# Performance work log

Measured on AMD Instinct MI355X. Metric: run time of the kernel, lower is better.

## Reference

```python
import jax, jax.numpy as jnp
import numpy as np

B, S, P, D = 32, 128, 64, 256   # batch, seq_len, pad_size, input_size
H, NF = 128, 3                   # hidden_size, n_filters
BI = 2                           # bidirectional -> b=2
OUT = 2                          # output_size
INITRANGE = 0.05


def setup_inputs() -> dict:
    key = jax.random.key(0)
    ks = jax.random.split(key, 17)
    u = lambda k, shape: jax.random.uniform(k, shape, jnp.float32, -INITRANGE, INITRANGE)
    return {
        "inputs": jax.random.normal(ks[0], (B, S, P, D), jnp.float32),
        "inputs_demoip": jax.random.normal(ks[1], (B, 3), jnp.float32),
        # Conv1d(1,1,kernel=D) collapses to a single dot product + scalar bias
        "conv_w": u(ks[2], (D,)),
        "conv_b": u(ks[3], ()),
        # Conv1d(1,NF,kernel=H*BI) collapses to NF dot products + bias
        "conv2_w": u(ks[4], (NF, H * BI)),
        "conv2_b": u(ks[5], (NF,)),
        # GRU params, forward and backward directions (PyTorch gate order r,z,n)
        "W_ih_f": u(ks[6], (3 * H, D)),
        "W_hh_f": u(ks[7], (3 * H, H)),
        "b_ih_f": u(ks[8], (3 * H,)),
        "b_hh_f": u(ks[9], (3 * H,)),
        "W_ih_b": u(ks[10], (3 * H, D)),
        "W_hh_b": u(ks[11], (3 * H, H)),
        "b_ih_b": u(ks[12], (3 * H,)),
        "b_hh_b": u(ks[13], (3 * H,)),
        "lin_w": u(ks[14], (OUT, H * BI * NF + 3)),
        "lin_b": u(ks[15], (OUT,)),
        "batch_size": B,
    }


def _gru_dir(x_seq, W_ih, W_hh, b_ih, b_hh, reverse):
    """Single-direction GRU, PyTorch semantics. x_seq: [B,S,D] -> [B,S,H]."""
    xg = jnp.einsum('bsd,gd->bsg', x_seq, W_ih) + b_ih  # [B,S,3H] precomputed input gates

    def step(h, xg_t):
        hg = h @ W_hh.T + b_hh
        xr, xz, xn = jnp.split(xg_t, 3, axis=-1)
        hr, hz, hn = jnp.split(hg, 3, axis=-1)
        r = jax.nn.sigmoid(xr + hr)
        z = jax.nn.sigmoid(xz + hz)
        n = jnp.tanh(xn + r * hn)
        h_new = (1.0 - z) * n + z * h
        return h_new, h_new

    h0 = jnp.zeros((x_seq.shape[0], W_hh.shape[1]), x_seq.dtype)
    _, hs = jax.lax.scan(step, h0, jnp.swapaxes(xg, 0, 1), reverse=reverse)
    return jnp.swapaxes(hs, 0, 1)


def reference(inputs, inputs_demoip, conv_w, conv_b, conv2_w, conv2_b,
              W_ih_f, W_hh_f, b_ih_f, b_hh_f,
              W_ih_b, W_hh_b, b_ih_b, b_hh_b,
              lin_w, lin_b, batch_size):
    # --- convolutional attention pooling over pad dim (fused, no per-step loop) ---
    scores = jnp.einsum('bspd,d->bsp', inputs, conv_w) + conv_b      # [B,S,P]
    conv_wts = jax.nn.softmax(scores, axis=-1)                        # [B,S,P]
    convolutions = jnp.einsum('bsp,bspd->bsd', conv_wts, inputs)      # [B,S,D]
    # --- bidirectional GRU (eval mode: dropout is identity) ---
    hf = _gru_dir(convolutions, W_ih_f, W_hh_f, b_ih_f, b_hh_f, False)
    hb = _gru_dir(convolutions, W_ih_b, W_hh_b, b_ih_b, b_hh_b, True)
    states_rnn = jnp.concatenate([hf, hb], axis=-1)                   # [B,S,2H]
    # --- second attention (conv2 over states, softmax over time per filter) ---
    alpha_scores = jnp.einsum('bsh,fh->bfs', states_rnn, conv2_w) + conv2_b[None, :, None]
    alpha = jax.nn.softmax(alpha_scores, axis=-1)                     # [B,NF,S]
    context = jnp.einsum('bfs,bsh->bfh', alpha, states_rnn).reshape(states_rnn.shape[0], -1)
    context_v2 = jnp.concatenate([context, inputs_demoip], axis=1)    # [B, 2H*NF+3]
    out = jax.nn.softmax(context_v2 @ lin_w.T + lin_b, axis=-1)       # [B,OUT]
    return out, alpha, states_rnn, context, conv_wts
```

## Files before the change

kernel.cpp:

```cpp
#include <hip/hip_runtime.h>
#include <hip/hip_bf16.h>

#define BB 32
#define SS 128
#define PP 64
#define DD 256
#define HH 128
#define NF 3


__global__ __launch_bounds__(256) void k_pool(
    const float* __restrict__ inp,
    const float* __restrict__ conv_w,
    const float* __restrict__ conv_bp,
    float* __restrict__ conv_out,
    float* __restrict__ conv_wts_out)
{
    __shared__ float scores[PP];
    __shared__ float wts[PP];
    __shared__ float4 part4[256];

    const int bs   = blockIdx.x;
    const int t    = threadIdx.x;
    const int lane = t & 63;
    const int wv   = t >> 6;

    const float4* src = reinterpret_cast<const float4*>(inp + (size_t)bs * (PP * DD));
    const float4  cw  = reinterpret_cast<const float4*>(conv_w)[lane];
    const float   cb  = conv_bp[0];

    float4 v[16];
#pragma unroll
    for (int i = 0; i < 16; ++i) v[i] = src[i * 256 + t];

    float part[16];
#pragma unroll
    for (int i = 0; i < 16; ++i)
        part[i] = v[i].x * cw.x + v[i].y * cw.y + v[i].z * cw.z + v[i].w * cw.w;

#pragma unroll
    for (int i = 0; i < 16; ++i) {
#pragma unroll
        for (int m = 32; m >= 1; m >>= 1) part[i] += __shfl_xor(part[i], m);
        if (lane == i) scores[i * 4 + wv] = part[i] + cb;
    }
    __syncthreads();

    if (wv == 0) {
        float s = scores[lane];
        float mx = s;
#pragma unroll
        for (int m = 32; m >= 1; m >>= 1) mx = fmaxf(mx, __shfl_xor(mx, m));
        float e = __expf(s - mx);
        float sm = e;
#pragma unroll
        for (int m = 32; m >= 1; m >>= 1) sm += __shfl_xor(sm, m);
        float w = e / sm;
        wts[lane] = w;
        conv_wts_out[(size_t)bs * PP + lane] = w;
    }
    __syncthreads();

    float4 acc = {0.f, 0.f, 0.f, 0.f};
#pragma unroll
    for (int i = 0; i < 16; ++i) {
        const float w = wts[4 * i + wv];
        acc.x = fmaf(w, v[i].x, acc.x);
        acc.y = fmaf(w, v[i].y, acc.y);
        acc.z = fmaf(w, v[i].z, acc.z);
        acc.w = fmaf(w, v[i].w, acc.w);
    }
    part4[t] = acc;
    __syncthreads();

    if (wv == 0) {
        float4 a = part4[lane];
        const float4 b1 = part4[64 + lane];
        const float4 b2 = part4[128 + lane];
        const float4 b3 = part4[192 + lane];
        a.x += b1.x + b2.x + b3.x;
        a.y += b1.y + b2.y + b3.y;
        a.z += b1.z + b2.z + b3.z;
        a.w += b1.w + b2.w + b3.w;
        reinterpret_cast<float4*>(conv_out + (size_t)bs * DD)[lane] = a;
    }
}

#define GBM 128
#define GBN 128
#define GBK 32
#define GAS 132

__global__ __launch_bounds__(256) void k_xg(
    const float* __restrict__ A,
    const float* __restrict__ Wf,
    const float* __restrict__ Wb,
    const float* __restrict__ bf,
    const float* __restrict__ bb,
    float* __restrict__ xg)
{
    __shared__ float as_[GBK * GAS];
    __shared__ float bs_[GBK * GAS];

    const int t  = threadIdx.x;
    const int i0 = blockIdx.x * GBM;
    const int j0 = blockIdx.y * GBN;
    const int tx = t & 15, ty = t >> 4;

    const float* Wsrc = (j0 < 384) ? (Wf + (size_t)j0 * DD) : (Wb + (size_t)(j0 - 384) * DD);
    const float* bsrc = (j0 < 384) ? (bf + j0) : (bb + (j0 - 384));

    float acc[8][8];
#pragma unroll
    for (int ii = 0; ii < 8; ++ii)
#pragma unroll
        for (int jj = 0; jj < 8; ++jj) acc[ii][jj] = 0.f;

    float4 pa[4], pb[4];
#pragma unroll
    for (int p = 0; p < 4; ++p) {
        const int idx = p * 256 + t, r = idx >> 3, k4 = idx & 7;
        pa[p] = *reinterpret_cast<const float4*>(&A[(size_t)(i0 + r) * DD + k4 * 4]);
        pb[p] = *reinterpret_cast<const float4*>(&Wsrc[(size_t)r * DD + k4 * 4]);
    }

    for (int kt = 0; kt < DD; kt += GBK) {
#pragma unroll
        for (int p = 0; p < 4; ++p) {
            const int idx = p * 256 + t, r = idx >> 3, k4 = idx & 7;
            as_[(k4 * 4 + 0) * GAS + r] = pa[p].x;
            as_[(k4 * 4 + 1) * GAS + r] = pa[p].y;
            as_[(k4 * 4 + 2) * GAS + r] = pa[p].z;
            as_[(k4 * 4 + 3) * GAS + r] = pa[p].w;
            bs_[(k4 * 4 + 0) * GAS + r] = pb[p].x;
            bs_[(k4 * 4 + 1) * GAS + r] = pb[p].y;
            bs_[(k4 * 4 + 2) * GAS + r] = pb[p].z;
            bs_[(k4 * 4 + 3) * GAS + r] = pb[p].w;
        }
        __syncthreads();
        if (kt + GBK < DD) {
#pragma unroll
            for (int p = 0; p < 4; ++p) {
                const int idx = p * 256 + t, r = idx >> 3, k4 = idx & 7;
                pa[p] = *reinterpret_cast<const float4*>(&A[(size_t)(i0 + r) * DD + kt + GBK + k4 * 4]);
                pb[p] = *reinterpret_cast<const float4*>(&Wsrc[(size_t)r * DD + kt + GBK + k4 * 4]);
            }
        }
#pragma unroll 8
        for (int k = 0; k < GBK; ++k) {
            float a[8], bq[8];
            *reinterpret_cast<float4*>(&a[0])  = *reinterpret_cast<const float4*>(&as_[k * GAS + ty * 8]);
            *reinterpret_cast<float4*>(&a[4])  = *reinterpret_cast<const float4*>(&as_[k * GAS + ty * 8 + 4]);
            *reinterpret_cast<float4*>(&bq[0]) = *reinterpret_cast<const float4*>(&bs_[k * GAS + tx * 4]);
            *reinterpret_cast<float4*>(&bq[4]) = *reinterpret_cast<const float4*>(&bs_[k * GAS + 64 + tx * 4]);
#pragma unroll
            for (int ii = 0; ii < 8; ++ii)
#pragma unroll
                for (int jj = 0; jj < 8; ++jj) acc[ii][jj] += a[ii] * bq[jj];
        }
        __syncthreads();
    }

    float bias[8];
#pragma unroll
    for (int jj = 0; jj < 4; ++jj) {
        bias[jj]     = bsrc[tx * 4 + jj];
        bias[4 + jj] = bsrc[64 + tx * 4 + jj];
    }
#pragma unroll
    for (int ii = 0; ii < 8; ++ii) {
        float* dst = &xg[(size_t)(i0 + ty * 8 + ii) * 768 + j0];
        float4 o0, o1;
        o0.x = acc[ii][0] + bias[0]; o0.y = acc[ii][1] + bias[1];
        o0.z = acc[ii][2] + bias[2]; o0.w = acc[ii][3] + bias[3];
        o1.x = acc[ii][4] + bias[4]; o1.y = acc[ii][5] + bias[5];
        o1.z = acc[ii][6] + bias[6]; o1.w = acc[ii][7] + bias[7];
        reinterpret_cast<float4*>(dst + tx * 4)[0]      = o0;
        reinterpret_cast<float4*>(dst + 64 + tx * 4)[0] = o1;
    }
}

__device__ __forceinline__ float sigm(float x) { return 1.f / (1.f + __expf(-x)); }
__device__ __forceinline__ float tanh_f(float x) { return 2.f / (1.f + __expf(-2.f * x)) - 1.f; }

template<int CTRL>
__device__ __forceinline__ float dpp_mov(float x) {
    return __int_as_float(__builtin_amdgcn_update_dpp(
        0, __float_as_int(x), CTRL, 0xF, 0xF, true));
}
#define DPP_XOR1 0xB1
#define DPP_XOR2 0x4E
#define DPP_HMIR 0x141

#define HSEG16 20
#define CH 16
#define XROW 384

__global__ __launch_bounds__(512) void k_gru(
    const float* __restrict__ xg,
    const float* __restrict__ Whf,
    const float* __restrict__ Whb,
    const float* __restrict__ bhf,
    const float* __restrict__ bhb,
    const float* __restrict__ c2w,
    float* __restrict__ states,
    float* __restrict__ sc_part)
{
    const int blk = blockIdx.x;
    const int b   = blk >> 1;
    const int dir = blk & 1;
    const int tid = threadIdx.x;
    const int g   = tid >> 3;
    const int p   = tid & 7;

    __shared__ float hb[2][8 * HSEG16];
    __shared__ float xs[2][CH * XROW];
    __shared__ float sring[2][CH][HH];

    const float* Wh = dir ? Whb : Whf;
    const float* bh = dir ? bhb : bhf;

    const int j = g + 64 * ((p >> 2) & 1);
    const bool gate = (p & 3) == 0;
    float bhr = 0.f, bhz = 0.f, bhn = 0.f;
    if (gate) { bhr = bh[j]; bhz = bh[HH + j]; bhn = bh[2 * HH + j]; }

    float4 wra[4], wrb[4], wza[4], wzb[4], wna[4], wnb[4];
    {
        const float4* p_ra = reinterpret_cast<const float4*>(Wh + (size_t)g * HH + p * 16);
        const float4* p_rb = reinterpret_cast<const float4*>(Wh + (size_t)(g + 64) * HH + p * 16);
        const float4* p_za = reinterpret_cast<const float4*>(Wh + (size_t)(HH + g) * HH + p * 16);
        const float4* p_zb = reinterpret_cast<const float4*>(Wh + (size_t)(HH + g + 64) * HH + p * 16);
        const float4* p_na = reinterpret_cast<const float4*>(Wh + (size_t)(2 * HH + g) * HH + p * 16);
        const float4* p_nb = reinterpret_cast<const float4*>(Wh + (size_t)(2 * HH + g + 64) * HH + p * 16);
#pragma unroll
        for (int k = 0; k < 4; ++k) {
            wra[k] = p_ra[k]; wrb[k] = p_rb[k];
            wza[k] = p_za[k]; wzb[k] = p_zb[k];
            wna[k] = p_na[k]; wnb[k] = p_nb[k];
        }
    }

    const float* xg_bd = xg + (size_t)b * SS * 768 + dir * 384;
    const int hidx = (j >> 4) * HSEG16 + (j & 15);

    float4 pf[3];
#pragma unroll
    for (int j3 = 0; j3 < 3; ++j3) {
        const int flat4 = j3 * 512 + tid;
        const int sic = flat4 / 96, w4 = flat4 % 96;
        const int s = dir ? (SS - 1 - sic) : sic;
        pf[j3] = *reinterpret_cast<const float4*>(xg_bd + (size_t)s * 768 + w4 * 4);
    }
#pragma unroll
    for (int j3 = 0; j3 < 3; ++j3) {
        const int flat4 = j3 * 512 + tid;
        const int sic = flat4 / 96, w4 = flat4 % 96;
        *reinterpret_cast<float4*>(&xs[0][sic * XROW + w4 * 4]) = pf[j3];
    }
    if (tid < 8 * HSEG16) hb[0][tid] = 0.f;
    __syncthreads();
#pragma unroll
    for (int j3 = 0; j3 < 3; ++j3) {
        const int flat4 = j3 * 512 + tid;
        const int sic = flat4 / 96, w4 = flat4 % 96;
        const int stp = CH + sic;
        const int s = dir ? (SS - 1 - stp) : stp;
        pf[j3] = *reinterpret_cast<const float4*>(xg_bd + (size_t)s * 768 + w4 * 4);
    }

    for (int step = 0; step < SS; ++step) {
        const int cur = step & 1;
        const int sic = step & (CH - 1);
        const int buf = (step >> 4) & 1;

        const float* hrow = hb[cur];
        float4 hq[4];
#pragma unroll
        for (int k = 0; k < 4; ++k)
            hq[k] = *reinterpret_cast<const float4*>(&hrow[p * HSEG16 + k * 4]);

        float hp = 0.f, xrv = 0.f, xzv = 0.f, xnv = 0.f;
        if (gate) {
            hp  = hrow[hidx];
            xrv = xs[buf][sic * XROW + j];
            xzv = xs[buf][sic * XROW + HH + j];
            xnv = xs[buf][sic * XROW + 2 * HH + j];
        }

        float a_ra = 0.f, a_rb = 0.f, a_za = 0.f, a_zb = 0.f, a_na = 0.f, a_nb = 0.f;
#pragma unroll
        for (int k = 0; k < 4; ++k) {
            const float4 h4 = hq[k];
            a_ra = fmaf(wra[k].x, h4.x, a_ra); a_ra = fmaf(wra[k].y, h4.y, a_ra);
            a_ra = fmaf(wra[k].z, h4.z, a_ra); a_ra = fmaf(wra[k].w, h4.w, a_ra);
            a_rb = fmaf(wrb[k].x, h4.x, a_rb); a_rb = fmaf(wrb[k].y, h4.y, a_rb);
            a_rb = fmaf(wrb[k].z, h4.z, a_rb); a_rb = fmaf(wrb[k].w, h4.w, a_rb);
            a_za = fmaf(wza[k].x, h4.x, a_za); a_za = fmaf(wza[k].y, h4.y, a_za);
            a_za = fmaf(wza[k].z, h4.z, a_za); a_za = fmaf(wza[k].w, h4.w, a_za);
            a_zb = fmaf(wzb[k].x, h4.x, a_zb); a_zb = fmaf(wzb[k].y, h4.y, a_zb);
            a_zb = fmaf(wzb[k].z, h4.z, a_zb); a_zb = fmaf(wzb[k].w, h4.w, a_zb);
            a_na = fmaf(wna[k].x, h4.x, a_na); a_na = fmaf(wna[k].y, h4.y, a_na);
            a_na = fmaf(wna[k].z, h4.z, a_na); a_na = fmaf(wna[k].w, h4.w, a_na);
            a_nb = fmaf(wnb[k].x, h4.x, a_nb); a_nb = fmaf(wnb[k].y, h4.y, a_nb);
            a_nb = fmaf(wnb[k].z, h4.z, a_nb); a_nb = fmaf(wnb[k].w, h4.w, a_nb);
        }

        const bool own_b = (tid & 4) != 0;
        const float s_r = own_b ? a_ra : a_rb;
        const float s_z = own_b ? a_za : a_zb;
        const float s_n = own_b ? a_na : a_nb;
        float f_r = (own_b ? a_rb : a_ra) + dpp_mov<DPP_HMIR>(s_r);
        float f_z = (own_b ? a_zb : a_za) + dpp_mov<DPP_HMIR>(s_z);
        float f_n = (own_b ? a_nb : a_na) + dpp_mov<DPP_HMIR>(s_n);
        f_r += dpp_mov<DPP_XOR1>(f_r);
        f_z += dpp_mov<DPP_XOR1>(f_z);
        f_n += dpp_mov<DPP_XOR1>(f_n);
        f_r += dpp_mov<DPP_XOR2>(f_r);
        f_z += dpp_mov<DPP_XOR2>(f_z);
        f_n += dpp_mov<DPP_XOR2>(f_n);

        if (gate) {
            const float r = sigm(xrv + f_r + bhr);
            const float z = sigm(xzv + f_z + bhz);
            const float n = tanh_f(xnv + r * (f_n + bhn));
            const float hnew = (1.f - z) * n + z * hp;
            hb[cur ^ 1][hidx] = hnew;
            sring[buf][sic][j] = hnew;
        }

        if (sic == CH - 1 && step != SS - 1) {
#pragma unroll
            for (int j3 = 0; j3 < 3; ++j3) {
                const int flat4 = j3 * 512 + tid;
                const int sc = flat4 / 96, w4 = flat4 % 96;
                *reinterpret_cast<float4*>(&xs[buf ^ 1][sc * XROW + w4 * 4]) = pf[j3];
            }
        }
        __syncthreads();

        if (sic == CH - 1) {
            const int cb = (step >> 4) * CH;
            {
                const int sic2 = tid >> 5;
                const int off  = (tid & 31) * 4;
                const int st   = cb + sic2;
                const int sO   = dir ? (SS - 1 - st) : st;
                const float4 v4 = *reinterpret_cast<const float4*>(&sring[buf][sic2][off]);
                *reinterpret_cast<float4*>(&states[((size_t)b * SS + sO) * 256 + dir * HH + off]) = v4;
            }
            if (tid < 384) {
                const int pair = tid >> 3;
                const int sl   = pair & 15;
                const int f    = pair >> 4;
                const int l8   = tid & 7;
                const float4* h4p = reinterpret_cast<const float4*>(&sring[buf][sl][l8 * 16]);
                const float4* w4p = reinterpret_cast<const float4*>(c2w + f * 256 + dir * HH + l8 * 16);
                float a = 0.f;
#pragma unroll
                for (int k = 0; k < 4; ++k) {
                    const float4 hv = h4p[k], wv4 = w4p[k];
                    a = fmaf(hv.x, wv4.x, a); a = fmaf(hv.y, wv4.y, a);
                    a = fmaf(hv.z, wv4.z, a); a = fmaf(hv.w, wv4.w, a);
                }
                a += dpp_mov<DPP_XOR1>(a);
                a += dpp_mov<DPP_XOR2>(a);
                a += dpp_mov<DPP_HMIR>(a);
                if (l8 == 0) {
                    const int st = cb + sl;
                    const int sO = dir ? (SS - 1 - st) : st;
                    sc_part[(((size_t)b * 2 + dir) * NF + f) * SS + sO] = a;
                }
            }
            if (step + CH + 1 < SS) {
                const int nchunk = (step >> 4) + 2;
#pragma unroll
                for (int j3 = 0; j3 < 3; ++j3) {
                    const int flat4 = j3 * 512 + tid;
                    const int sc = flat4 / 96, w4 = flat4 % 96;
                    const int st2 = nchunk * CH + sc;
                    const int s2 = dir ? (SS - 1 - st2) : st2;
                    pf[j3] = *reinterpret_cast<const float4*>(xg_bd + (size_t)s2 * 768 + w4 * 4);
                }
            }
        }
    }
}

__global__ __launch_bounds__(512) void k_attn2(
    const float* __restrict__ states,
    const float* __restrict__ sc_part,
    const float* __restrict__ c2b,
    const float* __restrict__ demoip,
    const float* __restrict__ lin_w,
    const float* __restrict__ lin_b,
    float* __restrict__ out,
    float* __restrict__ alpha_out,
    float* __restrict__ ctx_out)
{
    const int b    = blockIdx.x;
    const int t    = threadIdx.x;
    const int lane = t & 63;
    const int wv   = t >> 6;

    __shared__ float sc[NF * SS];
    __shared__ float al[NF * SS];
    __shared__ float pbuf[8][NF * 256];
    __shared__ float ctx[768];

    const float* st = states + (size_t)b * SS * 256;

    if (t < NF * SS) {
        const int f = t >> 7, s = t & 127;
        sc[t] = sc_part[(((size_t)b * 2 + 0) * NF + f) * SS + s]
              + sc_part[(((size_t)b * 2 + 1) * NF + f) * SS + s]
              + c2b[f];
    }
    __syncthreads();

    if (wv < NF) {
        const float v0 = sc[wv * SS + lane], v1 = sc[wv * SS + 64 + lane];
        float mx = fmaxf(v0, v1);
#pragma unroll
        for (int m = 32; m >= 1; m >>= 1) mx = fmaxf(mx, __shfl_xor(mx, m));
        const float e0 = __expf(v0 - mx), e1 = __expf(v1 - mx);
        float sm = e0 + e1;
#pragma unroll
        for (int m = 32; m >= 1; m >>= 1) sm += __shfl_xor(sm, m);
        const float r = 1.f / sm;
        al[wv * SS + lane]      = e0 * r;
        al[wv * SS + 64 + lane] = e1 * r;
        alpha_out[((size_t)b * NF + wv) * SS + lane]      = e0 * r;
        alpha_out[((size_t)b * NF + wv) * SS + 64 + lane] = e1 * r;
    }
    __syncthreads();

    {
        const int grp = t >> 6, h4 = t & 63;
        float4 c0 = {0,0,0,0}, c1 = {0,0,0,0}, c2 = {0,0,0,0};
#pragma unroll 4
        for (int i = 0; i < 16; ++i) {
            const int s = grp * 16 + i;
            const float4 sv = *reinterpret_cast<const float4*>(st + (size_t)s * 256 + h4 * 4);
            const float a0 = al[s], a1 = al[SS + s], a2 = al[2 * SS + s];
            c0.x = fmaf(a0, sv.x, c0.x); c0.y = fmaf(a0, sv.y, c0.y);
            c0.z = fmaf(a0, sv.z, c0.z); c0.w = fmaf(a0, sv.w, c0.w);
            c1.x = fmaf(a1, sv.x, c1.x); c1.y = fmaf(a1, sv.y, c1.y);
            c1.z = fmaf(a1, sv.z, c1.z); c1.w = fmaf(a1, sv.w, c1.w);
            c2.x = fmaf(a2, sv.x, c2.x); c2.y = fmaf(a2, sv.y, c2.y);
            c2.z = fmaf(a2, sv.z, c2.z); c2.w = fmaf(a2, sv.w, c2.w);
        }
        *reinterpret_cast<float4*>(&pbuf[grp][0 * 256 + h4 * 4]) = c0;
        *reinterpret_cast<float4*>(&pbuf[grp][1 * 256 + h4 * 4]) = c1;
        *reinterpret_cast<float4*>(&pbuf[grp][2 * 256 + h4 * 4]) = c2;
    }
    __syncthreads();

    for (int o = t; o < 768; o += 512) {
        float v = 0.f;
#pragma unroll
        for (int k = 0; k < 8; ++k) v += pbuf[k][o];
        ctx[o] = v;
        ctx_out[(size_t)b * 768 + o] = v;
    }
    __syncthreads();

    if (wv == 0) {
        const float* lw0 = lin_w;
        const float* lw1 = lin_w + 771;
        float a0 = 0.f, a1 = 0.f;
#pragma unroll 4
        for (int i = lane; i < 768; i += 64) {
            const float c = ctx[i];
            a0 = fmaf(c, lw0[i], a0);
            a1 = fmaf(c, lw1[i], a1);
        }
#pragma unroll
        for (int m = 32; m >= 1; m >>= 1) {
            a0 += __shfl_xor(a0, m);
            a1 += __shfl_xor(a1, m);
        }
        if (lane == 0) {
            a0 += lin_b[0]; a1 += lin_b[1];
            for (int k = 0; k < 3; ++k) {
                const float d = demoip[b * 3 + k];
                a0 = fmaf(d, lw0[768 + k], a0);
                a1 = fmaf(d, lw1[768 + k], a1);
            }
            const float m  = fmaxf(a0, a1);
            const float e0 = __expf(a0 - m), e1 = __expf(a1 - m);
            const float s  = e0 + e1;
            out[b * 2 + 0] = e0 / s;
            out[b * 2 + 1] = e1 / s;
        }
    }
}

extern "C" void kernel_launch(void* const* d_in, const int* in_sizes, int n_in,
                              void* d_out, int out_size, void* d_ws, size_t ws_size,
                              hipStream_t stream) {
    const float* inp     = (const float*)d_in[0];
    const float* demoip  = (const float*)d_in[1];
    const float* conv_w  = (const float*)d_in[2];
    const float* conv_b  = (const float*)d_in[3];
    const float* c2w     = (const float*)d_in[4];
    const float* c2b     = (const float*)d_in[5];
    const float* Wih_f   = (const float*)d_in[6];
    const float* Whh_f   = (const float*)d_in[7];
    const float* bih_f   = (const float*)d_in[8];
    const float* bhh_f   = (const float*)d_in[9];
    const float* Wih_b   = (const float*)d_in[10];
    const float* Whh_b   = (const float*)d_in[11];
    const float* bih_b   = (const float*)d_in[12];
    const float* bhh_b   = (const float*)d_in[13];
    const float* lin_w   = (const float*)d_in[14];
    const float* lin_b   = (const float*)d_in[15];

    float* out      = (float*)d_out;
    float* alpha    = out + 64;
    float* states   = out + 12352;
    float* context  = out + 1060928;
    float* conv_wts = out + 1085504;

    float* conv_out = (float*)d_ws;
    float* xg       = conv_out + (size_t)4096 * 256;
    float* sc_part  = conv_out;

    k_pool<<<dim3(BB * SS), dim3(256), 0, stream>>>(inp, conv_w, conv_b, conv_out, conv_wts);
    k_xg<<<dim3(4096 / GBM, 768 / GBN), dim3(256), 0, stream>>>(conv_out, Wih_f, Wih_b, bih_f, bih_b, xg);
    k_gru<<<dim3(64), dim3(512), 0, stream>>>(xg, Whh_f, Whh_b, bhh_f, bhh_b, c2w, states, sc_part);
    k_attn2<<<dim3(BB), dim3(512), 0, stream>>>(states, sc_part, c2b, demoip, lin_w, lin_b, out, alpha, context);
}
```

Measured before the change: 187.8 us.

## Repartition GRU recurrent matvec to 16 lanes per row group

Reworks the GRU hidden-state matvec decomposition. Each thread now covers 8 hidden inputs for 4 row groups per gate, with 16 partner lanes per group, where before it covered 16 inputs for 2 row groups with 8 lanes. The cross-lane reduction uses an extra DPP mirror stage, and the hidden-state shared buffer is padded in segments of 8. The aim is fewer LDS reads of h per step and shorter dependent FMA chains, in exchange for one more DPP reduction level per gate.

```diff
diff --git a/kernel.cpp b/kernel.cpp
--- a/kernel.cpp
+++ b/kernel.cpp
@@ -191,8 +191,9 @@
 #define DPP_XOR1 0xB1
 #define DPP_XOR2 0x4E
 #define DPP_HMIR 0x141
-
-#define HSEG16 20
+#define DPP_MIR  0x140
+
+#define HSEG8 12
 #define CH 16
 #define XROW 384
 
@@ -210,39 +211,36 @@
     const int b   = blk >> 1;
     const int dir = blk & 1;
     const int tid = threadIdx.x;
-    const int g   = tid >> 3;
-    const int p   = tid & 7;
-
-    __shared__ float hb[2][8 * HSEG16];
+    const int g4  = tid >> 4;
+    const int p   = tid & 15;
+
+    __shared__ float hb[2][16 * HSEG8];
     __shared__ float xs[2][CH * XROW];
     __shared__ float sring[2][CH][HH];
 
     const float* Wh = dir ? Whb : Whf;
     const float* bh = dir ? bhb : bhf;
 
-    const int j = g + 64 * ((p >> 2) & 1);
-    const bool gate = (p & 3) == 0;
+    const int  bit2 = (tid >> 2) & 1;
+    const int  bit3 = (tid >> 3) & 1;
+    const bool gate = (tid & 3) == 0;
+    const int  G    = 2 * bit2 + bit3;
+    const int  j    = g4 + 32 * G;
     float bhr = 0.f, bhz = 0.f, bhn = 0.f;
     if (gate) { bhr = bh[j]; bhz = bh[HH + j]; bhn = bh[2 * HH + j]; }
 
-    float4 wra[4], wrb[4], wza[4], wzb[4], wna[4], wnb[4];
-    {
-        const float4* p_ra = reinterpret_cast<const float4*>(Wh + (size_t)g * HH + p * 16);
-        const float4* p_rb = reinterpret_cast<const float4*>(Wh + (size_t)(g + 64) * HH + p * 16);
-        const float4* p_za = reinterpret_cast<const float4*>(Wh + (size_t)(HH + g) * HH + p * 16);
-        const float4* p_zb = reinterpret_cast<const float4*>(Wh + (size_t)(HH + g + 64) * HH + p * 16);
-        const float4* p_na = reinterpret_cast<const float4*>(Wh + (size_t)(2 * HH + g) * HH + p * 16);
-        const float4* p_nb = reinterpret_cast<const float4*>(Wh + (size_t)(2 * HH + g + 64) * HH + p * 16);
-#pragma unroll
-        for (int k = 0; k < 4; ++k) {
-            wra[k] = p_ra[k]; wrb[k] = p_rb[k];
-            wza[k] = p_za[k]; wzb[k] = p_zb[k];
-            wna[k] = p_na[k]; wnb[k] = p_nb[k];
-        }
-    }
+    float4 w[3][4][2];
+#pragma unroll
+    for (int q = 0; q < 3; ++q)
+#pragma unroll
+        for (int Gi = 0; Gi < 4; ++Gi) {
+            const float* row = Wh + (size_t)(q * HH + g4 + 32 * Gi) * HH + p * 8;
+            w[q][Gi][0] = *reinterpret_cast<const float4*>(row);
+            w[q][Gi][1] = *reinterpret_cast<const float4*>(row + 4);
+        }
 
     const float* xg_bd = xg + (size_t)b * SS * 768 + dir * 384;
-    const int hidx = (j >> 4) * HSEG16 + (j & 15);
+    const int hidx = (j >> 3) * HSEG8 + (j & 7);
 
     float4 pf[3];
 #pragma unroll
@@ -258,7 +256,7 @@
         const int sic = flat4 / 96, w4 = flat4 % 96;
         *reinterpret_cast<float4*>(&xs[0][sic * XROW + w4 * 4]) = pf[j3];
     }
-    if (tid < 8 * HSEG16) hb[0][tid] = 0.f;
+    if (tid < 16 * HSEG8) hb[0][tid] = 0.f;
     __syncthreads();
 #pragma unroll
     for (int j3 = 0; j3 < 3; ++j3) {
@@ -275,10 +273,8 @@
         const int buf = (step >> 4) & 1;
 
         const float* hrow = hb[cur];
-        float4 hq[4];
-#pragma unroll
-        for (int k = 0; k < 4; ++k)
-            hq[k] = *reinterpret_cast<const float4*>(&hrow[p * HSEG16 + k * 4]);
+        const float4 h0 = *reinterpret_cast<const float4*>(&hrow[p * HSEG8]);
+        const float4 h1 = *reinterpret_cast<const float4*>(&hrow[p * HSEG8 + 4]);
 
         float hp = 0.f, xrv = 0.f, xzv = 0.f, xnv = 0.f;
         if (gate) {
@@ -288,42 +284,40 @@
             xnv = xs[buf][sic * XROW + 2 * HH + j];
         }
 
-        float a_ra = 0.f, a_rb = 0.f, a_za = 0.f, a_zb = 0.f, a_na = 0.f, a_nb = 0.f;
-#pragma unroll
-        for (int k = 0; k < 4; ++k) {
-            const float4 h4 = hq[k];
-            a_ra = fmaf(wra[k].x, h4.x, a_ra); a_ra = fmaf(wra[k].y, h4.y, a_ra);
-            a_ra = fmaf(wra[k].z, h4.z, a_ra); a_ra = fmaf(wra[k].w, h4.w, a_ra);
-            a_rb = fmaf(wrb[k].x, h4.x, a_rb); a_rb = fmaf(wrb[k].y, h4.y, a_rb);
-            a_rb = fmaf(wrb[k].z, h4.z, a_rb); a_rb = fmaf(wrb[k].w, h4.w, a_rb);
-            a_za = fmaf(wza[k].x, h4.x, a_za); a_za = fmaf(wza[k].y, h4.y, a_za);
-            a_za = fmaf(wza[k].z, h4.z, a_za); a_za = fmaf(wza[k].w, h4.w, a_za);
-            a_zb = fmaf(wzb[k].x, h4.x, a_zb); a_zb = fmaf(wzb[k].y, h4.y, a_zb);
-            a_zb = fmaf(wzb[k].z, h4.z, a_zb); a_zb = fmaf(wzb[k].w, h4.w, a_zb);
-            a_na = fmaf(wna[k].x, h4.x, a_na); a_na = fmaf(wna[k].y, h4.y, a_na);
-            a_na = fmaf(wna[k].z, h4.z, a_na); a_na = fmaf(wna[k].w, h4.w, a_na);
-            a_nb = fmaf(wnb[k].x, h4.x, a_nb); a_nb = fmaf(wnb[k].y, h4.y, a_nb);
-            a_nb = fmaf(wnb[k].z, h4.z, a_nb); a_nb = fmaf(wnb[k].w, h4.w, a_nb);
-        }
-
-        const bool own_b = (tid & 4) != 0;
-        const float s_r = own_b ? a_ra : a_rb;
-        const float s_z = own_b ? a_za : a_zb;
-        const float s_n = own_b ? a_na : a_nb;
-        float f_r = (own_b ? a_rb : a_ra) + dpp_mov<DPP_HMIR>(s_r);
-        float f_z = (own_b ? a_zb : a_za) + dpp_mov<DPP_HMIR>(s_z);
-        float f_n = (own_b ? a_nb : a_na) + dpp_mov<DPP_HMIR>(s_n);
-        f_r += dpp_mov<DPP_XOR1>(f_r);
-        f_z += dpp_mov<DPP_XOR1>(f_z);
-        f_n += dpp_mov<DPP_XOR1>(f_n);
-        f_r += dpp_mov<DPP_XOR2>(f_r);
-        f_z += dpp_mov<DPP_XOR2>(f_z);
-        f_n += dpp_mov<DPP_XOR2>(f_n);
+        float a[3][4];
+#pragma unroll
+        for (int q = 0; q < 3; ++q)
+#pragma unroll
+            for (int Gi = 0; Gi < 4; ++Gi) {
+                float acc = 0.f;
+                acc = fmaf(w[q][Gi][0].x, h0.x, acc);
+                acc = fmaf(w[q][Gi][0].y, h0.y, acc);
+                acc = fmaf(w[q][Gi][0].z, h0.z, acc);
+                acc = fmaf(w[q][Gi][0].w, h0.w, acc);
+                acc = fmaf(w[q][Gi][1].x, h1.x, acc);
+                acc = fmaf(w[q][Gi][1].y, h1.y, acc);
+                acc = fmaf(w[q][Gi][1].z, h1.z, acc);
+                acc = fmaf(w[q][Gi][1].w, h1.w, acc);
+                a[q][Gi] = acc;
+            }
+
+        float F[3];
+#pragma unroll
+        for (int q = 0; q < 3; ++q) {
+            const float fA = (bit3 ? a[q][1] : a[q][0])
+                           + dpp_mov<DPP_MIR>(bit3 ? a[q][0] : a[q][1]);
+            const float fB = (bit3 ? a[q][3] : a[q][2])
+                           + dpp_mov<DPP_MIR>(bit3 ? a[q][2] : a[q][3]);
+            float f = (bit2 ? fB : fA) + dpp_mov<DPP_HMIR>(bit2 ? fA : fB);
+            f += dpp_mov<DPP_XOR1>(f);
+            f += dpp_mov<DPP_XOR2>(f);
+            F[q] = f;
+        }
 
         if (gate) {
-            const float r = sigm(xrv + f_r + bhr);
-            const float z = sigm(xzv + f_z + bhz);
-            const float n = tanh_f(xnv + r * (f_n + bhn));
+            const float r = sigm(xrv + F[0] + bhr);
+            const float z = sigm(xzv + F[1] + bhz);
+            const float n = tanh_f(xnv + r * (F[2] + bhn));
             const float hnew = (1.f - z) * n + z * hp;
             hb[cur ^ 1][hidx] = hnew;
             sring[buf][sic][j] = hnew;
@@ -356,20 +350,20 @@
                 const int l8   = tid & 7;
                 const float4* h4p = reinterpret_cast<const float4*>(&sring[buf][sl][l8 * 16]);
                 const float4* w4p = reinterpret_cast<const float4*>(c2w + f * 256 + dir * HH + l8 * 16);
-                float a = 0.f;
+                float aa = 0.f;
 #pragma unroll
                 for (int k = 0; k < 4; ++k) {
                     const float4 hv = h4p[k], wv4 = w4p[k];
-                    a = fmaf(hv.x, wv4.x, a); a = fmaf(hv.y, wv4.y, a);
-                    a = fmaf(hv.z, wv4.z, a); a = fmaf(hv.w, wv4.w, a);
+                    aa = fmaf(hv.x, wv4.x, aa); aa = fmaf(hv.y, wv4.y, aa);
+                    aa = fmaf(hv.z, wv4.z, aa); aa = fmaf(hv.w, wv4.w, aa);
                 }
-                a += dpp_mov<DPP_XOR1>(a);
-                a += dpp_mov<DPP_XOR2>(a);
-                a += dpp_mov<DPP_HMIR>(a);
+                aa += dpp_mov<DPP_XOR1>(aa);
+                aa += dpp_mov<DPP_XOR2>(aa);
+                aa += dpp_mov<DPP_HMIR>(aa);
                 if (l8 == 0) {
                     const int st = cb + sl;
                     const int sO = dir ? (SS - 1 - st) : st;
-                    sc_part[(((size_t)b * 2 + dir) * NF + f) * SS + sO] = a;
+                    sc_part[(((size_t)b * 2 + dir) * NF + f) * SS + sO] = aa;
                 }
             }
             if (step + CH + 1 < SS) {
```

Measured after the change: 203.4 us. +8.3%, slower.

## Compute input-gate projection with bf16 MFMA instead of fp32 SIMT GEMM

Applied to the files above, without the earlier changes.

The pooling kernel now writes its pooled activations as bf16. The input-gate GEMM is rewritten to convert each 16-row slice of W_ih to bf16 in LDS and run 16x16x32 bf16 MFMA instructions, reading A fragments straight from global memory. This replaces an fp32 register-tiled GEMM and halves the intermediate traffic, at the cost of bf16 rounding of the activations and weights feeding the GRU. Workspace offsets are rearranged so sc_part no longer aliases the pooled buffer.

```diff
diff --git a/kernel.cpp b/kernel.cpp
--- a/kernel.cpp
+++ b/kernel.cpp
@@ -9,11 +9,20 @@
 #define NF 3
 
 
+typedef __attribute__((ext_vector_type(8))) short short8v;
+typedef __attribute__((ext_vector_type(4))) float f32x4;
+
+__device__ __forceinline__ unsigned short f2bf(float x) {
+    unsigned int u = __float_as_uint(x);
+    u = (u + 0x7FFFu + ((u >> 16) & 1u)) >> 16;
+    return (unsigned short)u;
+}
+
 __global__ __launch_bounds__(256) void k_pool(
     const float* __restrict__ inp,
     const float* __restrict__ conv_w,
     const float* __restrict__ conv_bp,
-    float* __restrict__ conv_out,
+    unsigned short* __restrict__ conv_bf,
     float* __restrict__ conv_wts_out)
 {
     __shared__ float scores[PP];
@@ -82,102 +91,79 @@
         a.y += b1.y + b2.y + b3.y;
         a.z += b1.z + b2.z + b3.z;
         a.w += b1.w + b2.w + b3.w;
-        reinterpret_cast<float4*>(conv_out + (size_t)bs * DD)[lane] = a;
-    }
-}
-
-#define GBM 128
-#define GBN 128
-#define GBK 32
-#define GAS 132
+        ushort4 o;
+        o.x = f2bf(a.x); o.y = f2bf(a.y); o.z = f2bf(a.z); o.w = f2bf(a.w);
+        *reinterpret_cast<ushort4*>(conv_bf + (size_t)bs * DD + lane * 4) = o;
+    }
+}
+
+#define WLDS_P 264
 
 __global__ __launch_bounds__(256) void k_xg(
-    const float* __restrict__ A,
+    const unsigned short* __restrict__ conv_bf,
     const float* __restrict__ Wf,
     const float* __restrict__ Wb,
     const float* __restrict__ bf,
     const float* __restrict__ bb,
     float* __restrict__ xg)
 {
-    __shared__ float as_[GBK * GAS];
-    __shared__ float bs_[GBK * GAS];
+    __shared__ unsigned short wlds[16 * WLDS_P];
 
     const int t  = threadIdx.x;
-    const int i0 = blockIdx.x * GBM;
-    const int j0 = blockIdx.y * GBN;
-    const int tx = t & 15, ty = t >> 4;
-
-    const float* Wsrc = (j0 < 384) ? (Wf + (size_t)j0 * DD) : (Wb + (size_t)(j0 - 384) * DD);
-    const float* bsrc = (j0 < 384) ? (bf + j0) : (bb + (j0 - 384));
-
-    float acc[8][8];
-#pragma unroll
-    for (int ii = 0; ii < 8; ++ii)
-#pragma unroll
-        for (int jj = 0; jj < 8; ++jj) acc[ii][jj] = 0.f;
-
-    float4 pa[4], pb[4];
-#pragma unroll
-    for (int p = 0; p < 4; ++p) {
-        const int idx = p * 256 + t, r = idx >> 3, k4 = idx & 7;
-        pa[p] = *reinterpret_cast<const float4*>(&A[(size_t)(i0 + r) * DD + k4 * 4]);
-        pb[p] = *reinterpret_cast<const float4*>(&Wsrc[(size_t)r * DD + k4 * 4]);
-    }
-
-    for (int kt = 0; kt < DD; kt += GBK) {
-#pragma unroll
-        for (int p = 0; p < 4; ++p) {
-            const int idx = p * 256 + t, r = idx >> 3, k4 = idx & 7;
-            as_[(k4 * 4 + 0) * GAS + r] = pa[p].x;
-            as_[(k4 * 4 + 1) * GAS + r] = pa[p].y;
-            as_[(k4 * 4 + 2) * GAS + r] = pa[p].z;
-            as_[(k4 * 4 + 3) * GAS + r] = pa[p].w;
-            bs_[(k4 * 4 + 0) * GAS + r] = pb[p].x;
-            bs_[(k4 * 4 + 1) * GAS + r] = pb[p].y;
-            bs_[(k4 * 4 + 2) * GAS + r] = pb[p].z;
-            bs_[(k4 * 4 + 3) * GAS + r] = pb[p].w;
-        }
-        __syncthreads();
-        if (kt + GBK < DD) {
-#pragma unroll
-            for (int p = 0; p < 4; ++p) {
-                const int idx = p * 256 + t, r = idx >> 3, k4 = idx & 7;
-                pa[p] = *reinterpret_cast<const float4*>(&A[(size_t)(i0 + r) * DD + kt + GBK + k4 * 4]);
-                pb[p] = *reinterpret_cast<const float4*>(&Wsrc[(size_t)r * DD + kt + GBK + k4 * 4]);
-            }
-        }
-#pragma unroll 8
-        for (int k = 0; k < GBK; ++k) {
-            float a[8], bq[8];
-            *reinterpret_cast<float4*>(&a[0])  = *reinterpret_cast<const float4*>(&as_[k * GAS + ty * 8]);
-            *reinterpret_cast<float4*>(&a[4])  = *reinterpret_cast<const float4*>(&as_[k * GAS + ty * 8 + 4]);
-            *reinterpret_cast<float4*>(&bq[0]) = *reinterpret_cast<const float4*>(&bs_[k * GAS + tx * 4]);
-            *reinterpret_cast<float4*>(&bq[4]) = *reinterpret_cast<const float4*>(&bs_[k * GAS + 64 + tx * 4]);
-#pragma unroll
-            for (int ii = 0; ii < 8; ++ii)
-#pragma unroll
-                for (int jj = 0; jj < 8; ++jj) acc[ii][jj] += a[ii] * bq[jj];
-        }
-        __syncthreads();
-    }
-
-    float bias[8];
-#pragma unroll
-    for (int jj = 0; jj < 4; ++jj) {
-        bias[jj]     = bsrc[tx * 4 + jj];
-        bias[4 + jj] = bsrc[64 + tx * 4 + jj];
-    }
-#pragma unroll
-    for (int ii = 0; ii < 8; ++ii) {
-        float* dst = &xg[(size_t)(i0 + ty * 8 + ii) * 768 + j0];
-        float4 o0, o1;
-        o0.x = acc[ii][0] + bias[0]; o0.y = acc[ii][1] + bias[1];
-        o0.z = acc[ii][2] + bias[2]; o0.w = acc[ii][3] + bias[3];
-        o1.x = acc[ii][4] + bias[4]; o1.y = acc[ii][5] + bias[5];
-        o1.z = acc[ii][6] + bias[6]; o1.w = acc[ii][7] + bias[7];
-        reinterpret_cast<float4*>(dst + tx * 4)[0]      = o0;
-        reinterpret_cast<float4*>(dst + 64 + tx * 4)[0] = o1;
-    }
+    const int m0 = blockIdx.x * 256;
+    const int n0 = blockIdx.y * 16;
+
+    const float* Wsrc = (n0 < 384) ? (Wf + (size_t)n0 * DD) : (Wb + (size_t)(n0 - 384) * DD);
+    const float* bsrc = (n0 < 384) ? (bf + n0) : (bb + (n0 - 384));
+
+    {
+        const int n = t >> 4, kb = (t & 15) * 16;
+        const float4* src = reinterpret_cast<const float4*>(Wsrc + (size_t)n * DD + kb);
+        unsigned short tmp[16];
+#pragma unroll
+        for (int q = 0; q < 4; ++q) {
+            const float4 v = src[q];
+            tmp[q * 4 + 0] = f2bf(v.x);
+            tmp[q * 4 + 1] = f2bf(v.y);
+            tmp[q * 4 + 2] = f2bf(v.z);
+            tmp[q * 4 + 3] = f2bf(v.w);
+        }
+        unsigned short* dst = &wlds[n * WLDS_P + kb];
+        *reinterpret_cast<uint4*>(dst)     = *reinterpret_cast<uint4*>(&tmp[0]);
+        *reinterpret_cast<uint4*>(dst + 8) = *reinterpret_cast<uint4*>(&tmp[8]);
+    }
+    __syncthreads();
+
+    const int w    = t >> 6;
+    const int l    = t & 63;
+    const int lrow = l & 15;
+    const int lk8  = (l >> 4) * 8;
+
+    f32x4 acc[4];
+#pragma unroll
+    for (int mt = 0; mt < 4; ++mt) acc[mt] = (f32x4){0.f, 0.f, 0.f, 0.f};
+
+    const unsigned short* abase = conv_bf + (size_t)(m0 + w * 64 + lrow) * DD + lk8;
+    const unsigned short* bbase = &wlds[lrow * WLDS_P + lk8];
+
+#pragma unroll
+    for (int k0 = 0; k0 < DD; k0 += 32) {
+        const short8v bfrag = *reinterpret_cast<const short8v*>(bbase + k0);
+#pragma unroll
+        for (int mt = 0; mt < 4; ++mt) {
+            const short8v afrag = *reinterpret_cast<const short8v*>(abase + (size_t)mt * 16 * DD + k0);
+            acc[mt] = __builtin_amdgcn_mfma_f32_16x16x32_bf16(afrag, bfrag, acc[mt], 0, 0, 0);
+        }
+    }
+
+    const float bias_c = bsrc[lrow];
+    const int   col    = n0 + lrow;
+    const int   rbase  = m0 + w * 64 + (l >> 4) * 4;
+#pragma unroll
+    for (int mt = 0; mt < 4; ++mt)
+#pragma unroll
+        for (int r = 0; r < 4; ++r)
+            xg[(size_t)(rbase + mt * 16 + r) * 768 + col] = acc[mt][r] + bias_c;
 }
 
 __device__ __forceinline__ float sigm(float x) { return 1.f / (1.f + __expf(-x)); }
@@ -356,20 +342,20 @@
                 const int l8   = tid & 7;
                 const float4* h4p = reinterpret_cast<const float4*>(&sring[buf][sl][l8 * 16]);
                 const float4* w4p = reinterpret_cast<const float4*>(c2w + f * 256 + dir * HH + l8 * 16);
-                float a = 0.f;
+                float aa = 0.f;
 #pragma unroll
                 for (int k = 0; k < 4; ++k) {
                     const float4 hv = h4p[k], wv4 = w4p[k];
-                    a = fmaf(hv.x, wv4.x, a); a = fmaf(hv.y, wv4.y, a);
-                    a = fmaf(hv.z, wv4.z, a); a = fmaf(hv.w, wv4.w, a);
+                    aa = fmaf(hv.x, wv4.x, aa); aa = fmaf(hv.y, wv4.y, aa);
+                    aa = fmaf(hv.z, wv4.z, aa); aa = fmaf(hv.w, wv4.w, aa);
                 }
-                a += dpp_mov<DPP_XOR1>(a);
-                a += dpp_mov<DPP_XOR2>(a);
-                a += dpp_mov<DPP_HMIR>(a);
+                aa += dpp_mov<DPP_XOR1>(aa);
+                aa += dpp_mov<DPP_XOR2>(aa);
+                aa += dpp_mov<DPP_HMIR>(aa);
                 if (l8 == 0) {
                     const int st = cb + sl;
                     const int sO = dir ? (SS - 1 - st) : st;
-                    sc_part[(((size_t)b * 2 + dir) * NF + f) * SS + sO] = a;
+                    sc_part[(((size_t)b * 2 + dir) * NF + f) * SS + sO] = aa;
                 }
             }
             if (step + CH + 1 < SS) {
@@ -522,12 +508,13 @@
     float* context  = out + 1060928;
     float* conv_wts = out + 1085504;
 
-    float* conv_out = (float*)d_ws;
-    float* xg       = conv_out + (size_t)4096 * 256;
-    float* sc_part  = conv_out;
-
-    k_pool<<<dim3(BB * SS), dim3(256), 0, stream>>>(inp, conv_w, conv_b, conv_out, conv_wts);
-    k_xg<<<dim3(4096 / GBM, 768 / GBN), dim3(256), 0, stream>>>(conv_out, Wih_f, Wih_b, bih_f, bih_b, xg);
+    float* wsf            = (float*)d_ws;
+    unsigned short* cbf   = (unsigned short*)d_ws;
+    float* sc_part        = wsf + 524288;
+    float* xg             = wsf + 1048576;
+
+    k_pool<<<dim3(BB * SS), dim3(256), 0, stream>>>(inp, conv_w, conv_b, cbf, conv_wts);
+    k_xg<<<dim3(16, 48), dim3(256), 0, stream>>>(cbf, Wih_f, Wih_b, bih_f, bih_b, xg);
     k_gru<<<dim3(64), dim3(512), 0, stream>>>(xg, Whh_f, Whh_b, bhh_f, bhh_b, c2w, states, sc_part);
     k_attn2<<<dim3(BB), dim3(512), 0, stream>>>(states, sc_part, c2b, demoip, lin_w, lin_b, out, alpha, context);
 }
```

After: 163.8 us. 1.15x faster.
